# Kernel optimization log

Hardware: AMD Instinct MI355X
Metric: run time of the kernel (lower is better)

The kernel has to match this reference:

```python
import jax, jax.numpy as jnp
import numpy as np
from jax import lax
from jax.scipy.special import gammaln, logsumexp

BIG_NEG = -1e9


def _emission_log_probs(features, means, cov):
    # Diagonal Gaussian per class; the torch module stores cov as a (D,D) matrix
    # whose diagonal holds the (tied) variances (eye at init, torch.diag after fit),
    # and uses scale_tril = cov.sqrt() in a MultivariateNormal.
    var = jnp.diagonal(cov)                                  # (D,)
    D = features.shape[-1]
    x2 = (features ** 2) @ (1.0 / var)                       # (B,N)
    cross = features @ (means / var).T                       # (B,N,C)
    m2 = jnp.sum(means ** 2 / var, axis=-1)                  # (C,)
    quad = x2[..., None] - 2.0 * cross + m2                  # (B,N,C)
    logdet = jnp.sum(jnp.log(var))
    return -0.5 * (quad + logdet + D * jnp.log(2.0 * jnp.pi))


def _semi_markov_logZ(emission, lengths, trans, init, len_lp, K):
    # Semi-Markov CRF forward DP (partition function).
    # alpha[t,c] = logsumexp_{k=1..K, valid} beta[t-k,c] + span_emit(t-k,t,c) + len_lp[k-1,c]
    # beta[s,c]  = logsumexp_src alpha[s,src] + trans[c,src]   (beta[0,:] = init)
    B, N, C = emission.shape
    CE = jnp.concatenate([jnp.zeros((B, 1, C), emission.dtype), jnp.cumsum(emission, axis=1)], axis=1)  # (B,N+1,C)
    CEpad = jnp.concatenate([jnp.zeros((B, K, C), emission.dtype), CE], axis=1)  # (B,N+1+K,C)
    betapad = jnp.full((B, N + 1 + K, C), BIG_NEG, emission.dtype)
    betapad = betapad.at[:, K, :].set(jnp.broadcast_to(init, (B, C)))
    len_rev = len_lp[::-1]  # window slot j corresponds to span length K - j

    def step(bp, t):
        idx = t + K
        bw = lax.dynamic_slice(bp, (0, idx - K, 0), (B, K, C))       # beta[t-K..t-1]
        cew = lax.dynamic_slice(CEpad, (0, idx - K, 0), (B, K, C))   # cumsum at span starts
        ce_t = lax.dynamic_slice(CEpad, (0, idx, 0), (B, 1, C))      # cumsum at t
        span = ce_t - cew                                            # (B,K,C) span emission sums
        alpha_t = logsumexp(bw + span + len_rev[None], axis=1)       # (B,C)
        beta_t = logsumexp(alpha_t[:, None, :] + trans[None, :, :], axis=2)  # (B, tgt)
        bp = lax.dynamic_update_slice(bp, beta_t[:, None, :], (0, idx, 0))
        return bp, alpha_t

    _, alphas = lax.scan(step, betapad, jnp.arange(1, N + 1))
    alphas = jnp.transpose(alphas, (1, 0, 2))                        # (B,N,C)
    idx = (lengths - 1).astype(jnp.int32)[:, None, None]
    alpha_T = jnp.take_along_axis(alphas, jnp.broadcast_to(idx, (B, 1, C)), axis=1)[:, 0, :]
    return logsumexp(alpha_T, axis=-1)                               # (B,) log partition


def setup_inputs() -> dict:
    key = jax.random.key(0)
    ks = jax.random.split(key, 6)
    B, N, C, D, K = 32, 1024, 64, 512, 20
    features = jax.random.normal(ks[0], (B, N, D), jnp.float32)
    lengths = jnp.full((B,), N, dtype=jnp.int32)
    gaussian_means = 0.1 * jax.random.normal(ks[1], (C, D), jnp.float32)
    gaussian_cov = jnp.eye(D, dtype=jnp.float32)
    transition_logits = 0.1 * jax.random.normal(ks[2], (C, C), jnp.float32)
    init_logits = jax.random.uniform(ks[3], (C,), jnp.float32)
    poisson_log_rates = jnp.log(5.0) + 0.1 * jax.random.normal(ks[4], (C,), jnp.float32)
    return {"features": features, "lengths": lengths, "gaussian_means": gaussian_means,
            "gaussian_cov": gaussian_cov, "transition_logits": transition_logits,
            "init_logits": init_logits, "poisson_log_rates": poisson_log_rates, "max_k": K}


def reference(features, lengths, gaussian_means, gaussian_cov, transition_logits,
              init_logits, poisson_log_rates, max_k):
    C = gaussian_means.shape[0]
    emission = _emission_log_probs(features, gaussian_means, gaussian_cov)      # (B,N,C)
    # no self transitions: mask diagonal, column-normalize (trans[tgt,src] = log p(tgt|src))
    masked = jnp.where(jnp.eye(C, dtype=bool), BIG_NEG, transition_logits)
    trans = jax.nn.log_softmax(masked, axis=0)
    init = jax.nn.log_softmax(init_logits)
    kvals = jnp.arange(1, max_k + 1, dtype=features.dtype)
    len_lp = (kvals[:, None] * poisson_log_rates[None, :]
              - jnp.exp(poisson_log_rates)[None, :]
              - gammaln(kvals + 1.0)[:, None])                                  # (K,C) Poisson log-pmf
    return _semi_markov_logZ(emission, lengths, trans, init, len_lp, max_k)
```

## Files before the change

kernel.cpp:

```cpp
#include <hip/hip_runtime.h>
#include <math.h>

#define CC 64
#define KK 20
#define DCH 32
#define LOG2E 1.4426950408889634f
#define LN2   0.6931471805599453f
#define LN2PI 1.8378770664093453f
#define BIGN  -1.0e9f

#if __has_builtin(__builtin_amdgcn_exp2f)
#define EXP2(x) __builtin_amdgcn_exp2f(x)
#else
#define EXP2(x) exp2f(x)
#endif
#if __has_builtin(__builtin_amdgcn_logf)
#define LOG2(x) __builtin_amdgcn_logf(x)
#else
#define LOG2(x) log2f(x)
#endif

typedef float v2f __attribute__((ext_vector_type(2)));
typedef float v4f __attribute__((ext_vector_type(4)));

__device__ __forceinline__ v2f pk_fma(v2f a, v2f b, v2f c) {
  v2f d;
  asm("v_pk_fma_f32 %0, %1, %2, %3" : "=v"(d) : "v"(a), "v"(b), "v"(c));
  return d;
}

template <int Ctrl, int OldBits>
__device__ __forceinline__ float dpp_mov(float x) {
  return __int_as_float(__builtin_amdgcn_update_dpp(
      OldBits, __float_as_int(x), Ctrl, 0xf, 0xf, false));
}

__device__ __forceinline__ float wave_max64(float x) {
  constexpr int NI = (int)0xff800000;
  x = fmaxf(x, dpp_mov<0x111, NI>(x));
  x = fmaxf(x, dpp_mov<0x112, NI>(x));
  x = fmaxf(x, dpp_mov<0x114, NI>(x));
  x = fmaxf(x, dpp_mov<0x118, NI>(x));
  x = fmaxf(x, dpp_mov<0x142, NI>(x));
  x = fmaxf(x, dpp_mov<0x143, NI>(x));
  return __int_as_float(__builtin_amdgcn_readlane(__float_as_int(x), 63));
}

__device__ __forceinline__ float wave_sum64(float x) {
  x += dpp_mov<0x111, 0>(x);
  x += dpp_mov<0x112, 0>(x);
  x += dpp_mov<0x114, 0>(x);
  x += dpp_mov<0x118, 0>(x);
  x += dpp_mov<0x142, 0>(x);
  x += dpp_mov<0x143, 0>(x);
  return __int_as_float(__builtin_amdgcn_readlane(__float_as_int(x), 63));
}

__global__ void setup_kernel(const float* __restrict__ means,
                             const float* __restrict__ cov,
                             const float* __restrict__ tl,
                             const float* __restrict__ il,
                             const float* __restrict__ plr,
                             float* __restrict__ wmat,
                             float* __restrict__ invvar,
                             float* __restrict__ sinv,
                             float* __restrict__ q2,
                             float* __restrict__ P_T,
                             float* __restrict__ init2,
                             float* __restrict__ len2,
                             int D) {
  __shared__ float red[256];
  int tid = threadIdx.x;
  for (int d = tid; d < D; d += 256) {
    float v = 1.0f / cov[(size_t)d * D + d];
    invvar[d] = v;
    sinv[d] = sqrtf(v);
  }
  float lp_ = 0.f;
  for (int d = tid; d < D; d += 256) lp_ += logf(cov[(size_t)d * D + d]);
  red[tid] = lp_;
  __syncthreads();
  for (int s = 128; s > 0; s >>= 1) {
    if (tid < s) red[tid] += red[tid + s];
    __syncthreads();
  }
  float logdet = red[0];
  __syncthreads();
  {
    int c = tid & 63, q = tid >> 6;
    int dq = D / 4;
    float m2p = 0.f;
    for (int d = q * dq; d < (q + 1) * dq; ++d) {
      float mu = means[c * D + d];
      m2p = fmaf(mu * mu, invvar[d], m2p);
    }
    red[tid] = m2p;
  }
  __syncthreads();
  for (int i = tid; i < CC * D; i += 256) wmat[i] = means[i] * sinv[i % D];
  if (tid < CC) {
    int c = tid;
    float m2 = red[c] + red[c + 64] + red[c + 128] + red[c + 192];
    q2[c] = -0.5f * LOG2E * (m2 + logdet + (float)D * LN2PI);
    int j = c;
    float mx = -1e30f;
    for (int i2 = 0; i2 < CC; ++i2) {
      float v = (i2 == j) ? BIGN : tl[i2 * CC + j];
      mx = fmaxf(mx, v);
    }
    float s = 0.f;
    for (int i2 = 0; i2 < CC; ++i2) {
      float v = (i2 == j) ? BIGN : tl[i2 * CC + j];
      s += expf(v - mx);
    }
    float inv = 1.f / s;
    for (int i2 = 0; i2 < CC; ++i2) {
      float v = (i2 == j) ? BIGN : tl[i2 * CC + j];
      P_T[j * CC + i2] = expf(v - mx) * inv;
    }
    float mi = -1e30f;
    for (int i2 = 0; i2 < CC; ++i2) mi = fmaxf(mi, il[i2]);
    float si = 0.f;
    for (int i2 = 0; i2 < CC; ++i2) si += expf(il[i2] - mi);
    init2[c] = LOG2E * (il[c] - (mi + logf(si)));
  }
  for (int i = tid; i < KK * CC; i += 256) {
    int k = i / CC, c = i % CC;
    float lr = plr[c];
    float lp = (float)(k + 1) * lr - expf(lr) - lgammaf((float)(k + 2));
    len2[i] = LOG2E * lp;
  }
}

__global__ __launch_bounds__(256) void emission_kernel(
    const float* __restrict__ feat,
    const float* __restrict__ wmat,
    const float* __restrict__ sinv,
    const float* __restrict__ q2,
    float* __restrict__ emhat,
    float* __restrict__ kmax,
    int D) {
  __shared__ __align__(16) float xsT[DCH][68];
  __shared__ __align__(16) float wsT[DCH][68];
  __shared__ float q2s[CC];
  __shared__ float x2row[64];
  __shared__ float rmx[64][17];
  __shared__ float kapsh[64];
  int tid = threadIdx.x;
  size_t row0 = (size_t)blockIdx.x * 64;
  if (tid < CC) q2s[tid] = q2[tid];
  int lr_ = tid >> 2;
  int lq  = tid & 3;
  int lj  = lq * 8;
  int tx = tid & 15, ty = tid >> 4;
  int r0 = ty * 4, c0 = tx * 4;

  const float* fx = feat + (row0 + (size_t)lr_) * D + lj;
  const float* fw = wmat + (size_t)lr_ * D + lj;
  const float* fs = sinv + lj;

  float4 xa = *(const float4*)(fx);
  float4 xb = *(const float4*)(fx + 4);
  float4 wa = *(const float4*)(fw);
  float4 wb = *(const float4*)(fw + 4);
  float4 sa = *(const float4*)(fs);
  float4 sb = *(const float4*)(fs + 4);

  float acc[4][4] = {{0.f}};
  float x2p = 0.f;

  for (int d0 = 0; d0 < D; d0 += DCH) {
    __syncthreads();
    {
      float xs0 = xa.x * sa.x, xs1 = xa.y * sa.y, xs2 = xa.z * sa.z, xs3 = xa.w * sa.w;
      float xs4 = xb.x * sb.x, xs5 = xb.y * sb.y, xs6 = xb.z * sb.z, xs7 = xb.w * sb.w;
      xsT[lj + 0][lr_] = xs0; xsT[lj + 1][lr_] = xs1;
      xsT[lj + 2][lr_] = xs2; xsT[lj + 3][lr_] = xs3;
      xsT[lj + 4][lr_] = xs4; xsT[lj + 5][lr_] = xs5;
      xsT[lj + 6][lr_] = xs6; xsT[lj + 7][lr_] = xs7;
      wsT[lj + 0][lr_] = wa.x; wsT[lj + 1][lr_] = wa.y;
      wsT[lj + 2][lr_] = wa.z; wsT[lj + 3][lr_] = wa.w;
      wsT[lj + 4][lr_] = wb.x; wsT[lj + 5][lr_] = wb.y;
      wsT[lj + 6][lr_] = wb.z; wsT[lj + 7][lr_] = wb.w;
      x2p = fmaf(xs0, xs0, x2p); x2p = fmaf(xs1, xs1, x2p);
      x2p = fmaf(xs2, xs2, x2p); x2p = fmaf(xs3, xs3, x2p);
      x2p = fmaf(xs4, xs4, x2p); x2p = fmaf(xs5, xs5, x2p);
      x2p = fmaf(xs6, xs6, x2p); x2p = fmaf(xs7, xs7, x2p);
    }
    __syncthreads();
    if (d0 + DCH < D) {
      fx += DCH; fw += DCH; fs += DCH;
      xa = *(const float4*)(fx);
      xb = *(const float4*)(fx + 4);
      wa = *(const float4*)(fw);
      wb = *(const float4*)(fw + 4);
      sa = *(const float4*)(fs);
      sb = *(const float4*)(fs + 4);
    }
    #pragma unroll
    for (int j = 0; j < DCH; ++j) {
      float4 xv = *(const float4*)&xsT[j][r0];
      float4 wv = *(const float4*)&wsT[j][c0];
      acc[0][0] = fmaf(xv.x, wv.x, acc[0][0]);
      acc[0][1] = fmaf(xv.x, wv.y, acc[0][1]);
      acc[0][2] = fmaf(xv.x, wv.z, acc[0][2]);
      acc[0][3] = fmaf(xv.x, wv.w, acc[0][3]);
      acc[1][0] = fmaf(xv.y, wv.x, acc[1][0]);
      acc[1][1] = fmaf(xv.y, wv.y, acc[1][1]);
      acc[1][2] = fmaf(xv.y, wv.z, acc[1][2]);
      acc[1][3] = fmaf(xv.y, wv.w, acc[1][3]);
      acc[2][0] = fmaf(xv.z, wv.x, acc[2][0]);
      acc[2][1] = fmaf(xv.z, wv.y, acc[2][1]);
      acc[2][2] = fmaf(xv.z, wv.z, acc[2][2]);
      acc[2][3] = fmaf(xv.z, wv.w, acc[2][3]);
      acc[3][0] = fmaf(xv.w, wv.x, acc[3][0]);
      acc[3][1] = fmaf(xv.w, wv.y, acc[3][1]);
      acc[3][2] = fmaf(xv.w, wv.z, acc[3][2]);
      acc[3][3] = fmaf(xv.w, wv.w, acc[3][3]);
    }
  }

  x2p += dpp_mov<0xB1, 0>(x2p);
  x2p += dpp_mov<0x4E, 0>(x2p);
  if (lq == 0) x2row[lr_] = x2p;
  __syncthreads();

  float e[4][4];
  #pragma unroll
  for (int i = 0; i < 4; ++i) {
    float h = 0.5f * x2row[r0 + i];
    #pragma unroll
    for (int k2 = 0; k2 < 4; ++k2)
      e[i][k2] = LOG2E * (acc[i][k2] - h) + q2s[c0 + k2];
  }
  #pragma unroll
  for (int i = 0; i < 4; ++i)
    rmx[r0 + i][tx] = fmaxf(fmaxf(e[i][0], e[i][1]), fmaxf(e[i][2], e[i][3]));
  __syncthreads();
  if (tid < 64) {
    float m = rmx[tid][0];
    #pragma unroll
    for (int j = 1; j < 16; ++j) m = fmaxf(m, rmx[tid][j]);
    kapsh[tid] = m;
    kmax[row0 + tid] = m;
  }
  __syncthreads();
  #pragma unroll
  for (int i = 0; i < 4; ++i) {
    float kp = kapsh[r0 + i];
    size_t row = row0 + r0 + i;
    float4 o;
    o.x = EXP2(e[i][0] - kp); o.y = EXP2(e[i][1] - kp);
    o.z = EXP2(e[i][2] - kp); o.w = EXP2(e[i][3] - kp);
    *(float4*)&emhat[row * CC + c0] = o;
  }
}

__global__ __launch_bounds__(64, 1) void recur_kernel(
    const float* __restrict__ emhat,
    const float* __restrict__ kmax,
    const float* __restrict__ P_T,
    const float* __restrict__ init2,
    const float* __restrict__ len2,
    const int* __restrict__ lengths,
    float* __restrict__ out,
    int N) {
  __shared__ __align__(16) float abuf[CC];
  int b = blockIdx.x;
  int c = threadIdx.x;

  v2f P2[CC / 2];
  #pragma unroll
  for (int j = 0; j < CC / 2; ++j) {
    v2f p;
    p.x = P_T[(size_t)(2 * j) * CC + c];
    p.y = P_T[(size_t)(2 * j + 1) * CC + c];
    P2[j] = p;
  }
  float W[KK + 1];
  #pragma unroll
  for (int k = 1; k <= KK; ++k) W[k] = EXP2(len2[(k - 1) * CC + c]);
  float W1 = W[1];

  const float* eh_b = emhat + (size_t)b * N * CC;
  const float* km_b = kmax + (size_t)b * N;
  int len_b = lengths[b];

  float skp = 0.f;
  for (int r = c; r < len_b; r += 64) skp += km_b[r];
  float Skap = wave_sum64(skp);

  float v = EXP2(init2[c]);
  float rho = eh_b[c];
  float q0v = eh_b[(size_t)(1 <= N - 1 ? 1 : N - 1) * CC + c];
  float q1v = eh_b[(size_t)(2 <= N - 1 ? 2 : N - 1) * CC + c];
  float q2v = eh_b[(size_t)(3 <= N - 1 ? 3 : N - 1) * CC + c];
  float q3v = eh_b[(size_t)(4 <= N - 1 ? 4 : N - 1) * CC + c];
  float EfSum = 0.f;
  float A[KK];
  #pragma unroll
  for (int i = 0; i < KK; ++i) A[i] = 0.f;
  float rest = 0.f;

  auto matvec = [&](float a) -> float {
    abuf[c] = a;
    v2f a2[CC / 2];
    #pragma unroll
    for (int j = 0; j < CC / 4; ++j) {
      v4f t4 = *(v4f*)&abuf[4 * j];
      v2f lo, hi;
      lo.x = t4.x; lo.y = t4.y;
      hi.x = t4.z; hi.y = t4.w;
      a2[2 * j] = lo;
      a2[2 * j + 1] = hi;
    }
    v2f m0 = {0.f, 0.f}, m1 = {0.f, 0.f}, m2 = {0.f, 0.f}, m3 = {0.f, 0.f};
    #pragma unroll
    for (int j = 0; j < CC / 2; j += 4) {
      m0 = pk_fma(P2[j],     a2[j],     m0);
      m1 = pk_fma(P2[j + 1], a2[j + 1], m1);
      m2 = pk_fma(P2[j + 2], a2[j + 2], m2);
      m3 = pk_fma(P2[j + 3], a2[j + 3], m3);
    }
    return ((m0.x + m0.y) + (m1.x + m1.y)) + ((m2.x + m2.y) + (m3.x + m3.y));
  };

  auto body2 = [&](int t, float& qA, float& qB) {
    float A0a = v * rho;
    float aa = fmaf(A0a, W1, rest);

    abuf[c] = aa;
    v2f a2[CC / 2];
    #pragma unroll
    for (int j = 0; j < CC / 4; ++j) {
      v4f t4 = *(v4f*)&abuf[4 * j];
      v2f lo, hi;
      lo.x = t4.x; lo.y = t4.y;
      hi.x = t4.z; hi.y = t4.w;
      a2[2 * j] = lo;
      a2[2 * j + 1] = hi;
    }

    if (t == len_b) {
      float s_ = wave_sum64(aa);
      if (c == 0) out[b] = LN2 * (Skap + EfSum + LOG2(s_));
    }

    float d10 = 0.f, d11 = 0.f, d12 = 0.f, d13 = 0.f;
    #pragma unroll
    for (int i = 1; i + 3 <= 16; i += 4) {
      d10 = fmaf(A[i],     W[i + 2], d10);
      d11 = fmaf(A[i + 1], W[i + 3], d11);
      d12 = fmaf(A[i + 2], W[i + 4], d12);
      d13 = fmaf(A[i + 3], W[i + 5], d13);
    }
    d10 = fmaf(A[17], W[19], d10);
    d11 = fmaf(A[18], W[20], d11);
    float D1 = (d10 + d11) + (d12 + d13);

    float vmax = wave_max64(v);
    vmax = fminf(fmaxf(vmax, 1e-20f), 1e20f);
    int eb = (__float_as_int(vmax) >> 23) & 255;
    float scale = __int_as_float((254 - eb) << 23);
    EfSum += (float)(eb - 127);

    float rha = qA;
    int rowa = (t + 4 <= N - 1) ? (t + 4) : (N - 1);
    qA = eh_b[(size_t)rowa * CC + c];
    float rhon_a = rha * scale;

    float S2a = fmaf(A0a, W[2], D1);
    rest = rhon_a * S2a;

    {
      v2f m0 = {0.f, 0.f}, m1 = {0.f, 0.f}, m2 = {0.f, 0.f}, m3 = {0.f, 0.f};
      #pragma unroll
      for (int j = 0; j < CC / 2; j += 4) {
        m0 = pk_fma(P2[j],     a2[j],     m0);
        m1 = pk_fma(P2[j + 1], a2[j + 1], m1);
        m2 = pk_fma(P2[j + 2], a2[j + 2], m2);
        m3 = pk_fma(P2[j + 3], a2[j + 3], m3);
      }
      v = ((m0.x + m0.y) + (m1.x + m1.y)) + ((m2.x + m2.y) + (m3.x + m3.y));
    }

    float A0b = v * rhon_a;
    float ab = fmaf(A0b, W1, rest);

    abuf[c] = ab;
    v2f b2[CC / 2];
    #pragma unroll
    for (int j = 0; j < CC / 4; ++j) {
      v4f t4 = *(v4f*)&abuf[4 * j];
      v2f lo, hi;
      lo.x = t4.x; lo.y = t4.y;
      hi.x = t4.z; hi.y = t4.w;
      b2[2 * j] = lo;
      b2[2 * j + 1] = hi;
    }

    if (t + 1 == len_b) {
      float s_ = wave_sum64(ab);
      if (c == 0) out[b] = LN2 * (Skap + EfSum + LOG2(s_));
    }

    float d20 = 0.f, d21 = 0.f, d22 = 0.f, d23 = 0.f;
    #pragma unroll
    for (int i = 1; i + 3 <= 16; i += 4) {
      d20 = fmaf(A[i],     W[i + 3], d20);
      d21 = fmaf(A[i + 1], W[i + 4], d21);
      d22 = fmaf(A[i + 2], W[i + 5], d22);
      d23 = fmaf(A[i + 3], W[i + 6], d23);
    }
    d20 = fmaf(A[17], W[20], d20);
    float D2 = (d20 + d21) + (d22 + d23);

    float rhb = qB;
    int rowb = (t + 5 <= N - 1) ? (t + 5) : (N - 1);
    qB = eh_b[(size_t)rowb * CC + c];
    float rhon_b = rhb;

    float S2b = fmaf(A0b, W[2], rhon_a * fmaf(A0a, W[3], D2));
    rest = rhon_b * S2b;

    float r2 = rhon_a * rhon_b;
    #pragma unroll
    for (int i = 18; i >= 3; --i) A[i] = A[i - 2] * r2;
    A[2] = A0a * r2;
    A[1] = A0b * rhon_b;

    {
      v2f m0 = {0.f, 0.f}, m1 = {0.f, 0.f}, m2 = {0.f, 0.f}, m3 = {0.f, 0.f};
      #pragma unroll
      for (int j = 0; j < CC / 2; j += 4) {
        m0 = pk_fma(P2[j],     b2[j],     m0);
        m1 = pk_fma(P2[j + 1], b2[j + 1], m1);
        m2 = pk_fma(P2[j + 2], b2[j + 2], m2);
        m3 = pk_fma(P2[j + 3], b2[j + 3], m3);
      }
      v = ((m0.x + m0.y) + (m1.x + m1.y)) + ((m2.x + m2.y) + (m3.x + m3.y));
    }

    rho = rhon_b;
  };

  auto body1 = [&](int t, float& q) {
    float A0 = v * rho;
    float a = fmaf(A0, W1, rest);
    float vn = matvec(a);
    if (t == len_b) {
      float s_ = wave_sum64(a);
      if (c == 0) out[b] = LN2 * (Skap + EfSum + LOG2(s_));
    }
    float d10 = A0 * W[2], d11 = 0.f, d12 = 0.f, d13 = 0.f;
    #pragma unroll
    for (int i = 1; i + 3 <= 16; i += 4) {
      d10 = fmaf(A[i],     W[i + 2], d10);
      d11 = fmaf(A[i + 1], W[i + 3], d11);
      d12 = fmaf(A[i + 2], W[i + 4], d12);
      d13 = fmaf(A[i + 3], W[i + 5], d13);
    }
    d11 = fmaf(A[17], W[19], d11);
    d12 = fmaf(A[18], W[20], d12);
    float S2 = (d10 + d11) + (d12 + d13);
    float rh = q;
    int rown = (t + 4 <= N - 1) ? (t + 4) : (N - 1);
    q = eh_b[(size_t)rown * CC + c];
    float vmax = wave_max64(v);
    vmax = fminf(fmaxf(vmax, 1e-20f), 1e20f);
    int eb = (__float_as_int(vmax) >> 23) & 255;
    float scale = __int_as_float((254 - eb) << 23);
    EfSum += (float)(eb - 127);
    float rhon = rh * scale;
    rest = rhon * S2;
    #pragma unroll
    for (int i = 18; i >= 2; --i) A[i] = A[i - 1] * rhon;
    A[1] = A0 * rhon;
    v = vn;
    rho = rhon;
  };

  int t = 1;
  for (; t + 3 <= N; t += 4) {
    body2(t,     q0v, q1v);
    body2(t + 2, q2v, q3v);
  }
  for (; t <= N; ++t) {
    int s = t & 3;
    if (s == 1)      body1(t, q0v);
    else if (s == 2) body1(t, q1v);
    else if (s == 3) body1(t, q2v);
    else             body1(t, q3v);
  }
}

extern "C" void kernel_launch(void* const* d_in, const int* in_sizes, int n_in,
                              void* d_out, int out_size, void* d_ws, size_t ws_size,
                              hipStream_t stream) {
  const float* feat   = (const float*)d_in[0];
  const int*   lens   = (const int*)d_in[1];
  const float* means  = (const float*)d_in[2];
  const float* cov    = (const float*)d_in[3];
  const float* tl     = (const float*)d_in[4];
  const float* il     = (const float*)d_in[5];
  const float* plr    = (const float*)d_in[6];
  int B = in_sizes[1];
  int D = in_sizes[2] / CC;
  int N = in_sizes[0] / (B * D);

  float* ws = (float*)d_ws;
  size_t off = 0;
  float* wmat   = ws + off; off += (size_t)CC * D;
  float* invvar = ws + off; off += D;
  float* sinv   = ws + off; off += D;
  float* q2     = ws + off; off += CC;
  float* P_T    = ws + off; off += CC * CC;
  float* init2  = ws + off; off += CC;
  float* len2   = ws + off; off += KK * CC;
  float* emhat  = ws + off; off += (size_t)B * N * CC;
  float* kmax   = ws + off; off += (size_t)B * N;

  hipLaunchKernelGGL(setup_kernel, dim3(1), dim3(256), 0, stream,
                     means, cov, tl, il, plr, wmat, invvar, sinv, q2, P_T, init2, len2, D);
  hipLaunchKernelGGL(emission_kernel, dim3((B * N) / 64), dim3(256), 0, stream,
                     feat, wmat, sinv, q2, emhat, kmax, D);
  hipLaunchKernelGGL(recur_kernel, dim3(B), dim3(64), 0, stream,
                     emhat, kmax, P_T, init2, len2, lens, (float*)d_out, N);
}
```

Baseline: 465.3 us.

## Retile emission GEMM to 128-row blocks with 8x8 register tiles

The emission kernel now processes 128 rows per block with 128 threads, and each thread computes an 8x8 output tile instead of a 4x4 tile with 256 threads over 64 rows. Each thread loads a full row chunk of features and half a weight row, which changes global load patterns and increases register reuse per shared-memory read. The risk is higher register pressure (64 accumulators plus prefetch buffers), fewer blocks, and lower occupancy with launch_bounds(128,1). The total time is likely dominated by the sequential recurrence kernel, so this may matter little.

New measurement: 495.0 us. 1.06x slower.

```diff
diff --git a/kernel.cpp b/kernel.cpp
--- a/kernel.cpp
+++ b/kernel.cpp
@@ -4,6 +4,7 @@
 #define CC 64
 #define KK 20
 #define DCH 32
+#define EM_ROWS 128
 #define LOG2E 1.4426950408889634f
 #define LN2   0.6931471805599453f
 #define LN2PI 1.8378770664093453f
@@ -132,7 +133,7 @@
   }
 }
 
-__global__ __launch_bounds__(256) void emission_kernel(
+__global__ __launch_bounds__(128, 1) void emission_kernel(
     const float* __restrict__ feat,
     const float* __restrict__ wmat,
     const float* __restrict__ sinv,
@@ -140,119 +141,124 @@
     float* __restrict__ emhat,
     float* __restrict__ kmax,
     int D) {
-  __shared__ __align__(16) float xsT[DCH][68];
-  __shared__ __align__(16) float wsT[DCH][68];
+  __shared__ __align__(16) float xsT[DCH][EM_ROWS + 4];
+  __shared__ __align__(16) float wsT[DCH][CC + 4];
   __shared__ float q2s[CC];
-  __shared__ float x2row[64];
-  __shared__ float rmx[64][17];
-  __shared__ float kapsh[64];
+  __shared__ float x2sh[EM_ROWS];
+  __shared__ float rmx[EM_ROWS][9];
+  __shared__ float kapsh[EM_ROWS];
+
   int tid = threadIdx.x;
-  size_t row0 = (size_t)blockIdx.x * 64;
+  size_t row0 = (size_t)blockIdx.x * EM_ROWS;
   if (tid < CC) q2s[tid] = q2[tid];
-  int lr_ = tid >> 2;
-  int lq  = tid & 3;
-  int lj  = lq * 8;
-  int tx = tid & 15, ty = tid >> 4;
-  int r0 = ty * 4, c0 = tx * 4;
-
-  const float* fx = feat + (row0 + (size_t)lr_) * D + lj;
-  const float* fw = wmat + (size_t)lr_ * D + lj;
-  const float* fs = sinv + lj;
-
-  float4 xa = *(const float4*)(fx);
-  float4 xb = *(const float4*)(fx + 4);
-  float4 wa = *(const float4*)(fw);
-  float4 wb = *(const float4*)(fw + 4);
-  float4 sa = *(const float4*)(fs);
-  float4 sb = *(const float4*)(fs + 4);
-
-  float acc[4][4] = {{0.f}};
+  int tx = tid & 7;
+  int ty = tid >> 3;
+  int r0 = ty * 8, c0 = tx * 8;
+
+  const float* fx = feat + (row0 + (size_t)tid) * D;
+  int wc = tid >> 1;
+  int wh = (tid & 1) * 16;
+  const float* fw = wmat + (size_t)wc * D + wh;
+
+  float acc[8][8] = {{0.f}};
   float x2p = 0.f;
+
+  float4 px[8], pw[4];
+  #pragma unroll
+  for (int j4 = 0; j4 < 8; ++j4) px[j4] = *(const float4*)(fx + j4 * 4);
+  #pragma unroll
+  for (int j4 = 0; j4 < 4; ++j4) pw[j4] = *(const float4*)(fw + j4 * 4);
 
   for (int d0 = 0; d0 < D; d0 += DCH) {
     __syncthreads();
-    {
-      float xs0 = xa.x * sa.x, xs1 = xa.y * sa.y, xs2 = xa.z * sa.z, xs3 = xa.w * sa.w;
-      float xs4 = xb.x * sb.x, xs5 = xb.y * sb.y, xs6 = xb.z * sb.z, xs7 = xb.w * sb.w;
-      xsT[lj + 0][lr_] = xs0; xsT[lj + 1][lr_] = xs1;
-      xsT[lj + 2][lr_] = xs2; xsT[lj + 3][lr_] = xs3;
-      xsT[lj + 4][lr_] = xs4; xsT[lj + 5][lr_] = xs5;
-      xsT[lj + 6][lr_] = xs6; xsT[lj + 7][lr_] = xs7;
-      wsT[lj + 0][lr_] = wa.x; wsT[lj + 1][lr_] = wa.y;
-      wsT[lj + 2][lr_] = wa.z; wsT[lj + 3][lr_] = wa.w;
-      wsT[lj + 4][lr_] = wb.x; wsT[lj + 5][lr_] = wb.y;
-      wsT[lj + 6][lr_] = wb.z; wsT[lj + 7][lr_] = wb.w;
-      x2p = fmaf(xs0, xs0, x2p); x2p = fmaf(xs1, xs1, x2p);
-      x2p = fmaf(xs2, xs2, x2p); x2p = fmaf(xs3, xs3, x2p);
-      x2p = fmaf(xs4, xs4, x2p); x2p = fmaf(xs5, xs5, x2p);
-      x2p = fmaf(xs6, xs6, x2p); x2p = fmaf(xs7, xs7, x2p);
+    #pragma unroll
+    for (int j4 = 0; j4 < 8; ++j4) {
+      float s0 = sinv[d0 + j4 * 4 + 0];
+      float s1 = sinv[d0 + j4 * 4 + 1];
+      float s2 = sinv[d0 + j4 * 4 + 2];
+      float s3 = sinv[d0 + j4 * 4 + 3];
+      float a0 = px[j4].x * s0, a1 = px[j4].y * s1;
+      float a2 = px[j4].z * s2, a3 = px[j4].w * s3;
+      xsT[j4 * 4 + 0][tid] = a0;
+      xsT[j4 * 4 + 1][tid] = a1;
+      xsT[j4 * 4 + 2][tid] = a2;
+      xsT[j4 * 4 + 3][tid] = a3;
+      x2p = fmaf(a0, a0, x2p);
+      x2p = fmaf(a1, a1, x2p);
+      x2p = fmaf(a2, a2, x2p);
+      x2p = fmaf(a3, a3, x2p);
+    }
+    #pragma unroll
+    for (int j4 = 0; j4 < 4; ++j4) {
+      wsT[wh + j4 * 4 + 0][wc] = pw[j4].x;
+      wsT[wh + j4 * 4 + 1][wc] = pw[j4].y;
+      wsT[wh + j4 * 4 + 2][wc] = pw[j4].z;
+      wsT[wh + j4 * 4 + 3][wc] = pw[j4].w;
     }
     __syncthreads();
     if (d0 + DCH < D) {
-      fx += DCH; fw += DCH; fs += DCH;
-      xa = *(const float4*)(fx);
-      xb = *(const float4*)(fx + 4);
-      wa = *(const float4*)(fw);
-      wb = *(const float4*)(fw + 4);
-      sa = *(const float4*)(fs);
-      sb = *(const float4*)(fs + 4);
+      #pragma unroll
+      for (int j4 = 0; j4 < 8; ++j4)
+        px[j4] = *(const float4*)(fx + d0 + DCH + j4 * 4);
+      #pragma unroll
+      for (int j4 = 0; j4 < 4; ++j4)
+        pw[j4] = *(const float4*)(fw + d0 + DCH + j4 * 4);
     }
     #pragma unroll
     for (int j = 0; j < DCH; ++j) {
-      float4 xv = *(const float4*)&xsT[j][r0];
-      float4 wv = *(const float4*)&wsT[j][c0];
-      acc[0][0] = fmaf(xv.x, wv.x, acc[0][0]);
-      acc[0][1] = fmaf(xv.x, wv.y, acc[0][1]);
-      acc[0][2] = fmaf(xv.x, wv.z, acc[0][2]);
-      acc[0][3] = fmaf(xv.x, wv.w, acc[0][3]);
-      acc[1][0] = fmaf(xv.y, wv.x, acc[1][0]);
-      acc[1][1] = fmaf(xv.y, wv.y, acc[1][1]);
-      acc[1][2] = fmaf(xv.y, wv.z, acc[1][2]);
-      acc[1][3] = fmaf(xv.y, wv.w, acc[1][3]);
-      acc[2][0] = fmaf(xv.z, wv.x, acc[2][0]);
-      acc[2][1] = fmaf(xv.z, wv.y, acc[2][1]);
-      acc[2][2] = fmaf(xv.z, wv.z, acc[2][2]);
-      acc[2][3] = fmaf(xv.z, wv.w, acc[2][3]);
-      acc[3][0] = fmaf(xv.w, wv.x, acc[3][0]);
-      acc[3][1] = fmaf(xv.w, wv.y, acc[3][1]);
-      acc[3][2] = fmaf(xv.w, wv.z, acc[3][2]);
-      acc[3][3] = fmaf(xv.w, wv.w, acc[3][3]);
-    }
-  }
-
-  x2p += dpp_mov<0xB1, 0>(x2p);
-  x2p += dpp_mov<0x4E, 0>(x2p);
-  if (lq == 0) x2row[lr_] = x2p;
+      float4 xa = *(const float4*)&xsT[j][r0];
+      float4 xb = *(const float4*)&xsT[j][r0 + 4];
+      float4 wa = *(const float4*)&wsT[j][c0];
+      float4 wb = *(const float4*)&wsT[j][c0 + 4];
+      float xr[8] = {xa.x, xa.y, xa.z, xa.w, xb.x, xb.y, xb.z, xb.w};
+      float wr[8] = {wa.x, wa.y, wa.z, wa.w, wb.x, wb.y, wb.z, wb.w};
+      #pragma unroll
+      for (int r = 0; r < 8; ++r) {
+        #pragma unroll
+        for (int q = 0; q < 8; ++q)
+          acc[r][q] = fmaf(xr[r], wr[q], acc[r][q]);
+      }
+    }
+  }
+
+  x2sh[tid] = x2p;
   __syncthreads();
 
-  float e[4][4];
-  #pragma unroll
-  for (int i = 0; i < 4; ++i) {
-    float h = 0.5f * x2row[r0 + i];
-    #pragma unroll
-    for (int k2 = 0; k2 < 4; ++k2)
-      e[i][k2] = LOG2E * (acc[i][k2] - h) + q2s[c0 + k2];
-  }
-  #pragma unroll
-  for (int i = 0; i < 4; ++i)
-    rmx[r0 + i][tx] = fmaxf(fmaxf(e[i][0], e[i][1]), fmaxf(e[i][2], e[i][3]));
+  float e[8][8];
+  #pragma unroll
+  for (int r = 0; r < 8; ++r) {
+    float h = 0.5f * x2sh[r0 + r];
+    #pragma unroll
+    for (int q = 0; q < 8; ++q)
+      e[r][q] = LOG2E * (acc[r][q] - h) + q2s[c0 + q];
+  }
+  #pragma unroll
+  for (int r = 0; r < 8; ++r) {
+    float m = e[r][0];
+    #pragma unroll
+    for (int q = 1; q < 8; ++q) m = fmaxf(m, e[r][q]);
+    rmx[r0 + r][tx] = m;
+  }
   __syncthreads();
-  if (tid < 64) {
+  {
     float m = rmx[tid][0];
     #pragma unroll
-    for (int j = 1; j < 16; ++j) m = fmaxf(m, rmx[tid][j]);
+    for (int q = 1; q < 8; ++q) m = fmaxf(m, rmx[tid][q]);
     kapsh[tid] = m;
     kmax[row0 + tid] = m;
   }
   __syncthreads();
   #pragma unroll
-  for (int i = 0; i < 4; ++i) {
-    float kp = kapsh[r0 + i];
-    size_t row = row0 + r0 + i;
-    float4 o;
-    o.x = EXP2(e[i][0] - kp); o.y = EXP2(e[i][1] - kp);
-    o.z = EXP2(e[i][2] - kp); o.w = EXP2(e[i][3] - kp);
-    *(float4*)&emhat[row * CC + c0] = o;
+  for (int r = 0; r < 8; ++r) {
+    float kp = kapsh[r0 + r];
+    size_t row = row0 + r0 + r;
+    float4 o0, o1;
+    o0.x = EXP2(e[r][0] - kp); o0.y = EXP2(e[r][1] - kp);
+    o0.z = EXP2(e[r][2] - kp); o0.w = EXP2(e[r][3] - kp);
+    o1.x = EXP2(e[r][4] - kp); o1.y = EXP2(e[r][5] - kp);
+    o1.z = EXP2(e[r][6] - kp); o1.w = EXP2(e[r][7] - kp);
+    *(float4*)&emhat[row * CC + c0] = o0;
+    *(float4*)&emhat[row * CC + c0 + 4] = o1;
   }
 }
 
@@ -522,7 +528,7 @@
 
   hipLaunchKernelGGL(setup_kernel, dim3(1), dim3(256), 0, stream,
                      means, cov, tl, il, plr, wmat, invvar, sinv, q2, P_T, init2, len2, D);
-  hipLaunchKernelGGL(emission_kernel, dim3((B * N) / 64), dim3(256), 0, stream,
+  hipLaunchKernelGGL(emission_kernel, dim3((B * N) / EM_ROWS), dim3(128), 0, stream,
                      feat, wmat, sinv, q2, emhat, kmax, D);
   hipLaunchKernelGGL(recur_kernel, dim3(B), dim3(64), 0, stream,
                      emhat, kmax, P_T, init2, len2, lens, (float*)d_out, N);
```
